# Performance work log

Hardware: AMD Instinct MI355X
Metric: run time of the kernel (lower is better)

## Reference

```python
import jax, jax.numpy as jnp
import numpy as np

N_SRC = [700000, 51200, 5120]
N_DST = [51200, 5120, 1024]
N_EDGE = [768000, 51200, 5120]
IN_FEATS, N_HIDDEN, N_CLASSES = 128, 256, 47


def setup_inputs() -> dict:
    key = jax.random.key(0)
    ks = jax.random.split(key, 16)
    inp = {}
    inp["x"] = jax.random.normal(ks[0], (N_SRC[0], IN_FEATS), dtype=jnp.float32)
    # edge lists per block: src indexes block-src nodes, dst indexes block-dst nodes
    for l in range(3):
        inp[f"src{l}"] = jax.random.randint(ks[1 + 2 * l], (N_EDGE[l],), 0, N_SRC[l], dtype=jnp.int32)
        inp[f"dst{l}"] = jax.random.randint(ks[2 + 2 * l], (N_EDGE[l],), 0, N_DST[l], dtype=jnp.int32)
    dims = [(IN_FEATS, N_HIDDEN), (N_HIDDEN, N_HIDDEN), (N_HIDDEN, N_CLASSES)]
    for l, (di, do) in enumerate(dims):
        scale = 1.0 / np.sqrt(di)
        inp[f"Ws{l}"] = jax.random.normal(ks[7 + 3 * l], (di, do), dtype=jnp.float32) * scale
        inp[f"Wn{l}"] = jax.random.normal(ks[8 + 3 * l], (di, do), dtype=jnp.float32) * scale
        inp[f"b{l}"] = jnp.zeros((do,), dtype=jnp.float32)
    return inp


def _sage_conv(h, src, dst, n_dst, Ws, Wn, b):
    # mean-aggregate neighbor (src) features onto dst nodes, then dual linear
    h_dst = h[:n_dst]                                   # dst nodes are a prefix of src nodes
    msg = jax.ops.segment_sum(h[src], dst, num_segments=n_dst)
    deg = jax.ops.segment_sum(jnp.ones((src.shape[0], 1), h.dtype), dst, num_segments=n_dst)
    h_neigh = msg / jnp.maximum(deg, 1.0)               # zero-degree dst -> 0 (DGL convention)
    return h_dst @ Ws + h_neigh @ Wn + b


def reference(x, src0, dst0, src1, dst1, src2, dst2,
              Ws0, Wn0, b0, Ws1, Wn1, b1, Ws2, Wn2, b2):
    h = _sage_conv(x, src0, dst0, N_DST[0], Ws0, Wn0, b0)
    h = jax.nn.relu(h)  # dropout = identity in eval
    h = _sage_conv(h, src1, dst1, N_DST[1], Ws1, Wn1, b1)
    h = jax.nn.relu(h)
    h = _sage_conv(h, src2, dst2, N_DST[2], Ws2, Wn2, b2)
    return h
```

## Files before the change

kernel.cpp:

```cpp
#include <hip/hip_runtime.h>


typedef __bf16 bf16x8 __attribute__((ext_vector_type(8)));
typedef float f32x4 __attribute__((ext_vector_type(4)));

static __device__ __forceinline__ unsigned short f32_to_bf16(float f) {
    unsigned u = __float_as_uint(f);
    u += 0x7fffu + ((u >> 16) & 1u);
    return (unsigned short)(u >> 16);
}
static __device__ __forceinline__ float bf16lo(unsigned u) { return __uint_as_float(u << 16); }
static __device__ __forceinline__ float bf16hi(unsigned u) { return __uint_as_float(u & 0xffff0000u); }

__global__ void sage_prep(const float* __restrict__ x, unsigned short* __restrict__ xcast,
                          const float* __restrict__ Ws0, const float* __restrict__ Wn0,
                          const float* __restrict__ Ws1, const float* __restrict__ Wn1,
                          const float* __restrict__ Ws2, const float* __restrict__ Wn2,
                          unsigned short* __restrict__ WT0, unsigned short* __restrict__ WT1,
                          unsigned short* __restrict__ WT2,
                          const int* __restrict__ d0, int* __restrict__ c0,
                          const int* __restrict__ d1, int* __restrict__ c1,
                          const int* __restrict__ d2, int* __restrict__ c2) {
    const int b = blockIdx.x;
    if (b < 6400) {
        int i = b * 256 + threadIdx.x;
        float4 v = ((const float4*)x)[i];
        uint2 o;
        o.x = (unsigned)f32_to_bf16(v.x) | ((unsigned)f32_to_bf16(v.y) << 16);
        o.y = (unsigned)f32_to_bf16(v.z) | ((unsigned)f32_to_bf16(v.w) << 16);
        ((uint2*)xcast)[i] = o;
    } else if (b < 6656) {
        int idx = (b - 6400) * 256 + threadIdx.x;
        int n = idx >> 8, k = idx & 255;
        float v = (k < 128) ? Ws0[(size_t)k * 256 + n] : Wn0[(size_t)(k - 128) * 256 + n];
        WT0[idx] = f32_to_bf16(v);
    } else if (b < 7168) {
        int idx = (b - 6656) * 256 + threadIdx.x;
        int n = idx >> 9, k = idx & 511;
        float v = (k < 256) ? Ws1[(size_t)k * 256 + n] : Wn1[(size_t)(k - 256) * 256 + n];
        WT1[idx] = f32_to_bf16(v);
    } else if (b < 7262) {
        int idx = (b - 7168) * 256 + threadIdx.x;
        int n = idx >> 9, k = idx & 511;
        float v = (k < 256) ? Ws2[(size_t)k * 47 + n] : Wn2[(size_t)(k - 256) * 47 + n];
        WT2[idx] = f32_to_bf16(v);
    } else if (b < 10262) {
        atomicAdd(&c0[d0[(b - 7262) * 256 + threadIdx.x]], 1);
    } else if (b < 10462) {
        atomicAdd(&c1[d1[(b - 10262) * 256 + threadIdx.x]], 1);
    } else {
        atomicAdd(&c2[d2[(b - 10462) * 256 + threadIdx.x]], 1);
    }
}

__global__ void sage_scan(const int* __restrict__ c0, int* __restrict__ o0, int* __restrict__ u0,
                          const int* __restrict__ c1, int* __restrict__ o1, int* __restrict__ u1,
                          const int* __restrict__ c2, int* __restrict__ o2, int* __restrict__ u2) {
    const int* counts; int* offsets; int* cursor; int n;
    if (blockIdx.x == 0)      { counts = c0; offsets = o0; cursor = u0; n = 51200; }
    else if (blockIdx.x == 1) { counts = c1; offsets = o1; cursor = u1; n = 5120; }
    else                      { counts = c2; offsets = o2; cursor = u2; n = 1024; }

    __shared__ int wsum[16];
    __shared__ int wbase[16];
    __shared__ int s_carry;
    const int tid = threadIdx.x;
    const int lane = tid & 63;
    const int wid = tid >> 6;
    if (tid == 0) s_carry = 0;
    __syncthreads();

    for (int base = 0; base < n; base += 8192) {
        int idx = base + tid * 8;
        int v[8];
#pragma unroll
        for (int u = 0; u < 8; ++u) v[u] = (idx + u < n) ? counts[idx + u] : 0;
        int tsum = 0;
#pragma unroll
        for (int u = 0; u < 8; ++u) { int t = v[u]; v[u] = tsum; tsum += t; }
        int incl = tsum;
#pragma unroll
        for (int d = 1; d < 64; d <<= 1) {
            int t = __shfl_up(incl, d, 64);
            if (lane >= d) incl += t;
        }
        int wexcl = incl - tsum;
        if (lane == 63) wsum[wid] = incl;
        __syncthreads();
        int carry = s_carry;
        __syncthreads();
        if (tid < 64) {
            int s = (lane < 16) ? wsum[lane] : 0;
            int inc = s;
#pragma unroll
            for (int d = 1; d < 16; d <<= 1) {
                int t = __shfl_up(inc, d, 64);
                if (lane >= d) inc += t;
            }
            if (lane < 16) wbase[lane] = carry + inc - s;
            if (lane == 15) s_carry = carry + inc;
        }
        __syncthreads();
        int pre = wbase[wid] + wexcl;
#pragma unroll
        for (int u = 0; u < 8; ++u)
            if (idx + u < n) { int o = pre + v[u]; offsets[idx + u] = o; cursor[idx + u] = o; }
        __syncthreads();
    }
    if (tid == 0) offsets[n] = s_carry;
}

__global__ void sage_fill(const int* __restrict__ s0, const int* __restrict__ d0,
                          int* __restrict__ u0, int* __restrict__ r0,
                          const int* __restrict__ s1, const int* __restrict__ d1,
                          int* __restrict__ u1, int* __restrict__ r1,
                          const int* __restrict__ s2, const int* __restrict__ d2,
                          int* __restrict__ u2, int* __restrict__ r2) {
    const int b = blockIdx.x;
    if (b < 3000) {
        int i = b * 256 + threadIdx.x;
        int pos = atomicAdd(&u0[d0[i]], 1);
        r0[pos] = s0[i];
    } else if (b < 3200) {
        int i = (b - 3000) * 256 + threadIdx.x;
        int pos = atomicAdd(&u1[d1[i]], 1);
        r1[pos] = s1[i];
    } else {
        int i = (b - 3200) * 256 + threadIdx.x;
        int pos = atomicAdd(&u2[d2[i]], 1);
        r2[pos] = s2[i];
    }
}

__global__ void sage_gather0(const float* __restrict__ x, const int* __restrict__ csr,
                             const int* __restrict__ off, unsigned short* __restrict__ out,
                             int n_dst) {
    int row = (blockIdx.x * 256 + threadIdx.x) >> 6;
    if (row >= n_dst) return;
    const int lane = threadIdx.x & 63;
    const int half = lane >> 5;
    const int fl = lane & 31;
    const int beg = off[row], end = off[row + 1];
    const float4* hp = (const float4*)x + fl;
    float4 accA = make_float4(0.f, 0.f, 0.f, 0.f);
    float4 accB = make_float4(0.f, 0.f, 0.f, 0.f);
    int i = beg;
    for (; i + 7 < end; i += 8) {
        int s0 = csr[i + half];
        int s1 = csr[i + 2 + half];
        int s2 = csr[i + 4 + half];
        int s3 = csr[i + 6 + half];
        float4 v0 = hp[(size_t)s0 * 32];
        float4 v1 = hp[(size_t)s1 * 32];
        float4 v2 = hp[(size_t)s2 * 32];
        float4 v3 = hp[(size_t)s3 * 32];
        accA.x += v0.x; accA.y += v0.y; accA.z += v0.z; accA.w += v0.w;
        accB.x += v1.x; accB.y += v1.y; accB.z += v1.z; accB.w += v1.w;
        accA.x += v2.x; accA.y += v2.y; accA.z += v2.z; accA.w += v2.w;
        accB.x += v3.x; accB.y += v3.y; accB.z += v3.z; accB.w += v3.w;
    }
    for (; i + 1 < end; i += 2) {
        int s = csr[i + half];
        float4 v = hp[(size_t)s * 32];
        accA.x += v.x; accA.y += v.y; accA.z += v.z; accA.w += v.w;
    }
    if (i < end && half == 0) {
        int s = csr[i];
        float4 v = hp[(size_t)s * 32];
        accA.x += v.x; accA.y += v.y; accA.z += v.z; accA.w += v.w;
    }
    accA.x += accB.x; accA.y += accB.y; accA.z += accB.z; accA.w += accB.w;
    accA.x += __shfl_down(accA.x, 32);
    accA.y += __shfl_down(accA.y, 32);
    accA.z += __shfl_down(accA.z, 32);
    accA.w += __shfl_down(accA.w, 32);
    if (half == 0) {
        float inv = 1.0f / fmaxf((float)(end - beg), 1.0f);
        uint2 o;
        o.x = (unsigned)f32_to_bf16(accA.x * inv) | ((unsigned)f32_to_bf16(accA.y * inv) << 16);
        o.y = (unsigned)f32_to_bf16(accA.z * inv) | ((unsigned)f32_to_bf16(accA.w * inv) << 16);
        ((uint2*)out)[(size_t)row * 32 + fl] = o;
    }
}

__global__ void sage_gather256(const unsigned short* __restrict__ h, const int* __restrict__ csr,
                               const int* __restrict__ off, unsigned short* __restrict__ out,
                               int n_dst) {
    int row = (blockIdx.x * 256 + threadIdx.x) >> 6;
    if (row >= n_dst) return;
    const int lane = threadIdx.x & 63;
    const int half = lane >> 5;
    const int fl = lane & 31;
    const int beg = off[row], end = off[row + 1];
    const uint4* hp = (const uint4*)h + fl;
    float a[8] = {0.f, 0.f, 0.f, 0.f, 0.f, 0.f, 0.f, 0.f};
    float b[8] = {0.f, 0.f, 0.f, 0.f, 0.f, 0.f, 0.f, 0.f};
    int i = beg;
    for (; i + 3 < end; i += 4) {
        int s0 = csr[i + half];
        int s1 = csr[i + 2 + half];
        uint4 u0 = hp[(size_t)s0 * 32];
        uint4 u1 = hp[(size_t)s1 * 32];
        a[0] += bf16lo(u0.x); a[1] += bf16hi(u0.x);
        a[2] += bf16lo(u0.y); a[3] += bf16hi(u0.y);
        a[4] += bf16lo(u0.z); a[5] += bf16hi(u0.z);
        a[6] += bf16lo(u0.w); a[7] += bf16hi(u0.w);
        b[0] += bf16lo(u1.x); b[1] += bf16hi(u1.x);
        b[2] += bf16lo(u1.y); b[3] += bf16hi(u1.y);
        b[4] += bf16lo(u1.z); b[5] += bf16hi(u1.z);
        b[6] += bf16lo(u1.w); b[7] += bf16hi(u1.w);
    }
    for (; i + 1 < end; i += 2) {
        int s = csr[i + half];
        uint4 u = hp[(size_t)s * 32];
        a[0] += bf16lo(u.x); a[1] += bf16hi(u.x);
        a[2] += bf16lo(u.y); a[3] += bf16hi(u.y);
        a[4] += bf16lo(u.z); a[5] += bf16hi(u.z);
        a[6] += bf16lo(u.w); a[7] += bf16hi(u.w);
    }
    if (i < end && half == 0) {
        int s = csr[i];
        uint4 u = hp[(size_t)s * 32];
        a[0] += bf16lo(u.x); a[1] += bf16hi(u.x);
        a[2] += bf16lo(u.y); a[3] += bf16hi(u.y);
        a[4] += bf16lo(u.z); a[5] += bf16hi(u.z);
        a[6] += bf16lo(u.w); a[7] += bf16hi(u.w);
    }
#pragma unroll
    for (int k = 0; k < 8; ++k) { a[k] += b[k]; a[k] += __shfl_down(a[k], 32); }
    if (half == 0) {
        float inv = 1.0f / fmaxf((float)(end - beg), 1.0f);
        uint4 o;
        o.x = (unsigned)f32_to_bf16(a[0] * inv) | ((unsigned)f32_to_bf16(a[1] * inv) << 16);
        o.y = (unsigned)f32_to_bf16(a[2] * inv) | ((unsigned)f32_to_bf16(a[3] * inv) << 16);
        o.z = (unsigned)f32_to_bf16(a[4] * inv) | ((unsigned)f32_to_bf16(a[5] * inv) << 16);
        o.w = (unsigned)f32_to_bf16(a[6] * inv) | ((unsigned)f32_to_bf16(a[7] * inv) << 16);
        ((uint4*)out)[(size_t)row * 32 + fl] = o;
    }
}

template <int RELU, int OUT_BF16>
__launch_bounds__(256)
__global__ void sage_gemm(const unsigned short* __restrict__ Hdst,
                          const unsigned short* __restrict__ Hneigh,
                          const unsigned short* __restrict__ WT,
                          const float* __restrict__ bias,
                          void* __restrict__ Out,
                          int N, int K1) {
    const int Ktot = 2 * K1;
    __shared__ unsigned short smem[2][128][72];
    unsigned short (*As)[72] = smem[0];
    unsigned short (*Bs)[72] = smem[1];

    const int t = threadIdx.x;
    const int lane = t & 63;
    const int w = t >> 6;
    const int wm = (w >> 1) * 64;
    const int wn = (w & 1) * 64;
    const int bm = blockIdx.y * 128;
    const int bn = blockIdx.x * 128;

    const int rowL = t >> 1;
    const int kL = (t & 1) * 32;

    f32x4 acc[4][4] = {};

    const int ktiles = Ktot >> 6;
    for (int kt = 0; kt < ktiles; ++kt) {
        const int k0 = kt << 6;
        {
            const unsigned short* src = (k0 < K1)
                ? (Hdst + (size_t)(bm + rowL) * K1 + k0 + kL)
                : (Hneigh + (size_t)(bm + rowL) * K1 + (k0 - K1) + kL);
            uint4 v0 = *(const uint4*)src;
            uint4 v1 = *(const uint4*)(src + 8);
            uint4 v2 = *(const uint4*)(src + 16);
            uint4 v3 = *(const uint4*)(src + 24);
            *(uint4*)&As[rowL][kL]      = v0;
            *(uint4*)&As[rowL][kL + 8]  = v1;
            *(uint4*)&As[rowL][kL + 16] = v2;
            *(uint4*)&As[rowL][kL + 24] = v3;
        }
        {
            int n = bn + rowL;
            uint4 v0 = {0,0,0,0}, v1 = {0,0,0,0}, v2 = {0,0,0,0}, v3 = {0,0,0,0};
            if (n < N) {
                const unsigned short* srcB = WT + (size_t)n * Ktot + k0 + kL;
                v0 = *(const uint4*)srcB;
                v1 = *(const uint4*)(srcB + 8);
                v2 = *(const uint4*)(srcB + 16);
                v3 = *(const uint4*)(srcB + 24);
            }
            *(uint4*)&Bs[rowL][kL]      = v0;
            *(uint4*)&Bs[rowL][kL + 8]  = v1;
            *(uint4*)&Bs[rowL][kL + 16] = v2;
            *(uint4*)&Bs[rowL][kL + 24] = v3;
        }
        __syncthreads();

        const int fr = lane & 15;
        const int fk = (lane >> 4) * 8;
#pragma unroll
        for (int ks = 0; ks < 64; ks += 32) {
            bf16x8 av[4], bv[4];
#pragma unroll
            for (int mt = 0; mt < 4; ++mt) av[mt] = *(const bf16x8*)&As[wm + mt * 16 + fr][ks + fk];
#pragma unroll
            for (int nt = 0; nt < 4; ++nt) bv[nt] = *(const bf16x8*)&Bs[wn + nt * 16 + fr][ks + fk];
#pragma unroll
            for (int mt = 0; mt < 4; ++mt)
#pragma unroll
                for (int nt = 0; nt < 4; ++nt)
                    acc[mt][nt] = __builtin_amdgcn_mfma_f32_16x16x32_bf16(av[mt], bv[nt], acc[mt][nt], 0, 0, 0);
        }
        __syncthreads();
    }

    const int quad = lane >> 4;
    const int colL = lane & 15;
    if (OUT_BF16 && N == 256) {
        unsigned short* C = (unsigned short*)smem;
#pragma unroll
        for (int mt = 0; mt < 4; ++mt)
#pragma unroll
            for (int nt = 0; nt < 4; ++nt)
#pragma unroll
                for (int r = 0; r < 4; ++r) {
                    int lrow = wm + mt * 16 + quad * 4 + r;
                    int lcol = wn + nt * 16 + colL;
                    float v = acc[mt][nt][r] + bias[bn + lcol];
                    if (RELU) v = fmaxf(v, 0.0f);
                    C[lrow * 136 + lcol] = f32_to_bf16(v);
                }
        __syncthreads();
        unsigned short* o = (unsigned short*)Out;
#pragma unroll
        for (int c = 0; c < 8; ++c) {
            int chunk = t * 8 + c;
            int row = chunk >> 4, cc = chunk & 15;
            uint4 v = *(const uint4*)&C[row * 136 + cc * 8];
            *(uint4*)(o + (size_t)(bm + row) * N + bn + cc * 8) = v;
        }
    } else {
#pragma unroll
        for (int mt = 0; mt < 4; ++mt)
#pragma unroll
            for (int nt = 0; nt < 4; ++nt)
#pragma unroll
                for (int r = 0; r < 4; ++r) {
                    int grow = bm + wm + mt * 16 + quad * 4 + r;
                    int gcol = bn + wn + nt * 16 + colL;
                    if (gcol < N) {
                        float v = acc[mt][nt][r] + bias[gcol];
                        if (RELU) v = fmaxf(v, 0.0f);
                        if (OUT_BF16) ((unsigned short*)Out)[(size_t)grow * N + gcol] = f32_to_bf16(v);
                        else ((float*)Out)[(size_t)grow * N + gcol] = v;
                    }
                }
    }
}


extern "C" void kernel_launch(void* const* d_in, const int* in_sizes, int n_in,
                              void* d_out, int out_size, void* d_ws, size_t ws_size,
                              hipStream_t stream) {
    const float* x    = (const float*)d_in[0];
    const int* src0 = (const int*)d_in[1];
    const int* dst0 = (const int*)d_in[2];
    const int* src1 = (const int*)d_in[3];
    const int* dst1 = (const int*)d_in[4];
    const int* src2 = (const int*)d_in[5];
    const int* dst2 = (const int*)d_in[6];
    const float* Ws0 = (const float*)d_in[7];
    const float* Wn0 = (const float*)d_in[8];
    const float* b0  = (const float*)d_in[9];
    const float* Ws1 = (const float*)d_in[10];
    const float* Wn1 = (const float*)d_in[11];
    const float* b1  = (const float*)d_in[12];
    const float* Ws2 = (const float*)d_in[13];
    const float* Wn2 = (const float*)d_in[14];
    const float* b2  = (const float*)d_in[15];
    float* out = (float*)d_out;

    char* ws = (char*)d_ws;
    unsigned short* xcast   = (unsigned short*)(ws + 0);
    unsigned short* h1      = (unsigned short*)(ws + 13107200);
    unsigned short* h2      = (unsigned short*)(ws + 39321600);
    unsigned short* hneigh0 = (unsigned short*)(ws + 41943040);
    unsigned short* hneigh1 = (unsigned short*)(ws + 55050240);
    unsigned short* hneigh2 = (unsigned short*)(ws + 57671680);
    unsigned short* WT0     = (unsigned short*)(ws + 58195968);
    unsigned short* WT1     = (unsigned short*)(ws + 58327040);
    unsigned short* WT2     = (unsigned short*)(ws + 58589184);
    int* counts0 = (int*)(ws + 58637312);
    int* counts1 = (int*)(ws + 58842112);
    int* counts2 = (int*)(ws + 58862592);
    int* off0    = (int*)(ws + 58866688);
    int* off1    = (int*)(ws + 59071504);
    int* off2    = (int*)(ws + 59092000);
    int* cur0    = (int*)(ws + 59096112);
    int* cur1    = (int*)(ws + 59300912);
    int* cur2    = (int*)(ws + 59321392);
    int* csr0    = (int*)(ws + 59325488);
    int* csr1    = (int*)(ws + 62397488);
    int* csr2    = (int*)(ws + 62602288);

    hipMemsetAsync(counts0, 0, 229376, stream);

    sage_prep<<<10482, 256, 0, stream>>>(x, xcast, Ws0, Wn0, Ws1, Wn1, Ws2, Wn2,
                                         WT0, WT1, WT2,
                                         dst0, counts0, dst1, counts1, dst2, counts2);
    sage_scan<<<3, 1024, 0, stream>>>(counts0, off0, cur0, counts1, off1, cur1, counts2, off2, cur2);
    sage_fill<<<3220, 256, 0, stream>>>(src0, dst0, cur0, csr0,
                                        src1, dst1, cur1, csr1,
                                        src2, dst2, cur2, csr2);

    sage_gather0<<<12800, 256, 0, stream>>>(x, csr0, off0, hneigh0, 51200);
    { dim3 g(2, 400); sage_gemm<1, 1><<<g, 256, 0, stream>>>(xcast, hneigh0, WT0, b0, h1, 256, 128); }

    sage_gather256<<<1280, 256, 0, stream>>>(h1, csr1, off1, hneigh1, 5120);
    { dim3 g(2, 40); sage_gemm<1, 1><<<g, 256, 0, stream>>>(h1, hneigh1, WT1, b1, h2, 256, 256); }

    sage_gather256<<<256, 256, 0, stream>>>(h2, csr2, off2, hneigh2, 1024);
    { dim3 g(1, 8); sage_gemm<0, 0><<<g, 256, 0, stream>>>(h2, hneigh2, WT2, b2, out, 47, 256); }
}
```

Baseline: 720.0 us.

## Parallelize CSR scan across blocks with atomic sync and vectorize edge loads

The three-block serial prefix scan becomes a 56-block scan. Each block scans 1024 counts, publishes its total through a global sync array, spins until all blocks arrive, then adds the totals of the blocks before it. The count and fill kernels also process two edges per thread using int2 loads, which halves their block counts. The spin barrier assumes all 56 blocks are resident at the same time, which holds on this GPU but is not guaranteed in general.

```diff
diff --git a/kernel.cpp b/kernel.cpp
--- a/kernel.cpp
+++ b/kernel.cpp
@@ -44,70 +44,87 @@
         int n = idx >> 9, k = idx & 511;
         float v = (k < 256) ? Ws2[(size_t)k * 47 + n] : Wn2[(size_t)(k - 256) * 47 + n];
         WT2[idx] = f32_to_bf16(v);
-    } else if (b < 10262) {
-        atomicAdd(&c0[d0[(b - 7262) * 256 + threadIdx.x]], 1);
-    } else if (b < 10462) {
-        atomicAdd(&c1[d1[(b - 10262) * 256 + threadIdx.x]], 1);
+    } else if (b < 8762) {
+        int i = (b - 7262) * 256 + threadIdx.x;
+        int2 d = ((const int2*)d0)[i];
+        atomicAdd(&c0[d.x], 1);
+        atomicAdd(&c0[d.y], 1);
+    } else if (b < 8862) {
+        int i = (b - 8762) * 256 + threadIdx.x;
+        int2 d = ((const int2*)d1)[i];
+        atomicAdd(&c1[d.x], 1);
+        atomicAdd(&c1[d.y], 1);
     } else {
-        atomicAdd(&c2[d2[(b - 10462) * 256 + threadIdx.x]], 1);
-    }
-}
-
+        int i = (b - 8862) * 256 + threadIdx.x;
+        int2 d = ((const int2*)d2)[i];
+        atomicAdd(&c2[d.x], 1);
+        atomicAdd(&c2[d.y], 1);
+    }
+}
+
+__launch_bounds__(1024)
 __global__ void sage_scan(const int* __restrict__ c0, int* __restrict__ o0, int* __restrict__ u0,
                           const int* __restrict__ c1, int* __restrict__ o1, int* __restrict__ u1,
-                          const int* __restrict__ c2, int* __restrict__ o2, int* __restrict__ u2) {
-    const int* counts; int* offsets; int* cursor; int n;
-    if (blockIdx.x == 0)      { counts = c0; offsets = o0; cursor = u0; n = 51200; }
-    else if (blockIdx.x == 1) { counts = c1; offsets = o1; cursor = u1; n = 5120; }
-    else                      { counts = c2; offsets = o2; cursor = u2; n = 1024; }
-
-    __shared__ int wsum[16];
-    __shared__ int wbase[16];
-    __shared__ int s_carry;
+                          const int* __restrict__ c2, int* __restrict__ o2, int* __restrict__ u2,
+                          int* __restrict__ sync) {
+    const int b = blockIdx.x;
     const int tid = threadIdx.x;
     const int lane = tid & 63;
     const int wid = tid >> 6;
-    if (tid == 0) s_carry = 0;
+    const int* counts; int* off; int* cur; int chunk, first, nblk, n;
+    if (b < 50)      { counts = c0; off = o0; cur = u0; chunk = b;      first = 0;  nblk = 50; n = 51200; }
+    else if (b < 55) { counts = c1; off = o1; cur = u1; chunk = b - 50; first = 50; nblk = 5;  n = 5120;  }
+    else             { counts = c2; off = o2; cur = u2; chunk = 0;      first = 55; nblk = 1;  n = 1024;  }
+
+    const int idx = chunk * 1024 + tid;
+    const int v = counts[idx];
+
+    int incl = v;
+#pragma unroll
+    for (int d = 1; d < 64; d <<= 1) {
+        int t = __shfl_up(incl, d, 64);
+        if (lane >= d) incl += t;
+    }
+
+    __shared__ int wsum[16];
+    __shared__ int s_base;
+    if (lane == 63) wsum[wid] = incl;
     __syncthreads();
 
-    for (int base = 0; base < n; base += 8192) {
-        int idx = base + tid * 8;
-        int v[8];
-#pragma unroll
-        for (int u = 0; u < 8; ++u) v[u] = (idx + u < n) ? counts[idx + u] : 0;
-        int tsum = 0;
-#pragma unroll
-        for (int u = 0; u < 8; ++u) { int t = v[u]; v[u] = tsum; tsum += t; }
-        int incl = tsum;
-#pragma unroll
-        for (int d = 1; d < 64; d <<= 1) {
-            int t = __shfl_up(incl, d, 64);
-            if (lane >= d) incl += t;
-        }
-        int wexcl = incl - tsum;
-        if (lane == 63) wsum[wid] = incl;
-        __syncthreads();
-        int carry = s_carry;
-        __syncthreads();
-        if (tid < 64) {
-            int s = (lane < 16) ? wsum[lane] : 0;
-            int inc = s;
-#pragma unroll
-            for (int d = 1; d < 16; d <<= 1) {
-                int t = __shfl_up(inc, d, 64);
-                if (lane >= d) inc += t;
-            }
-            if (lane < 16) wbase[lane] = carry + inc - s;
-            if (lane == 15) s_carry = carry + inc;
-        }
-        __syncthreads();
-        int pre = wbase[wid] + wexcl;
-#pragma unroll
-        for (int u = 0; u < 8; ++u)
-            if (idx + u < n) { int o = pre + v[u]; offsets[idx + u] = o; cursor[idx + u] = o; }
-        __syncthreads();
-    }
-    if (tid == 0) offsets[n] = s_carry;
+    if (tid < 64) {
+        int s = (lane < 16) ? wsum[lane] : 0;
+        int inc = s;
+#pragma unroll
+        for (int d = 1; d < 16; d <<= 1) {
+            int t = __shfl_up(inc, d, 64);
+            if (lane >= d) inc += t;
+        }
+        if (lane < 16) wsum[lane] = inc - s;
+        if (lane == 15) {
+            __hip_atomic_store(&sync[16 + b], inc, __ATOMIC_RELEASE, __HIP_MEMORY_SCOPE_AGENT);
+            __hip_atomic_fetch_add(&sync[0], 1, __ATOMIC_RELEASE, __HIP_MEMORY_SCOPE_AGENT);
+        }
+    }
+    if (tid == 0) {
+        while (__hip_atomic_load(&sync[0], __ATOMIC_ACQUIRE, __HIP_MEMORY_SCOPE_AGENT) < 56)
+            __builtin_amdgcn_s_sleep(2);
+    }
+    __syncthreads();
+
+    if (tid < 64) {
+        int p = (lane < chunk)
+            ? __hip_atomic_load(&sync[16 + first + lane], __ATOMIC_RELAXED, __HIP_MEMORY_SCOPE_AGENT)
+            : 0;
+#pragma unroll
+        for (int d = 32; d >= 1; d >>= 1) p += __shfl_down(p, d, 64);
+        if (lane == 0) s_base = p;
+    }
+    __syncthreads();
+
+    const int excl = s_base + wsum[wid] + (incl - v);
+    off[idx] = excl;
+    cur[idx] = excl;
+    if (chunk == nblk - 1 && tid == 1023) off[n] = excl + v;
 }
 
 __global__ void sage_fill(const int* __restrict__ s0, const int* __restrict__ d0,
@@ -117,18 +134,30 @@
                           const int* __restrict__ s2, const int* __restrict__ d2,
                           int* __restrict__ u2, int* __restrict__ r2) {
     const int b = blockIdx.x;
-    if (b < 3000) {
+    if (b < 1500) {
         int i = b * 256 + threadIdx.x;
-        int pos = atomicAdd(&u0[d0[i]], 1);
-        r0[pos] = s0[i];
-    } else if (b < 3200) {
-        int i = (b - 3000) * 256 + threadIdx.x;
-        int pos = atomicAdd(&u1[d1[i]], 1);
-        r1[pos] = s1[i];
+        int2 s = ((const int2*)s0)[i];
+        int2 d = ((const int2*)d0)[i];
+        int p0 = atomicAdd(&u0[d.x], 1);
+        int p1 = atomicAdd(&u0[d.y], 1);
+        r0[p0] = s.x;
+        r0[p1] = s.y;
+    } else if (b < 1600) {
+        int i = (b - 1500) * 256 + threadIdx.x;
+        int2 s = ((const int2*)s1)[i];
+        int2 d = ((const int2*)d1)[i];
+        int p0 = atomicAdd(&u1[d.x], 1);
+        int p1 = atomicAdd(&u1[d.y], 1);
+        r1[p0] = s.x;
+        r1[p1] = s.y;
     } else {
-        int i = (b - 3200) * 256 + threadIdx.x;
-        int pos = atomicAdd(&u2[d2[i]], 1);
-        r2[pos] = s2[i];
+        int i = (b - 1600) * 256 + threadIdx.x;
+        int2 s = ((const int2*)s2)[i];
+        int2 d = ((const int2*)d2)[i];
+        int p0 = atomicAdd(&u2[d.x], 1);
+        int p1 = atomicAdd(&u2[d.y], 1);
+        r2[p0] = s.x;
+        r2[p1] = s.y;
     }
 }
 
@@ -395,23 +424,25 @@
     int* counts0 = (int*)(ws + 58637312);
     int* counts1 = (int*)(ws + 58842112);
     int* counts2 = (int*)(ws + 58862592);
-    int* off0    = (int*)(ws + 58866688);
-    int* off1    = (int*)(ws + 59071504);
-    int* off2    = (int*)(ws + 59092000);
-    int* cur0    = (int*)(ws + 59096112);
-    int* cur1    = (int*)(ws + 59300912);
-    int* cur2    = (int*)(ws + 59321392);
-    int* csr0    = (int*)(ws + 59325488);
-    int* csr1    = (int*)(ws + 62397488);
-    int* csr2    = (int*)(ws + 62602288);
-
-    hipMemsetAsync(counts0, 0, 229376, stream);
-
-    sage_prep<<<10482, 256, 0, stream>>>(x, xcast, Ws0, Wn0, Ws1, Wn1, Ws2, Wn2,
-                                         WT0, WT1, WT2,
-                                         dst0, counts0, dst1, counts1, dst2, counts2);
-    sage_scan<<<3, 1024, 0, stream>>>(counts0, off0, cur0, counts1, off1, cur1, counts2, off2, cur2);
-    sage_fill<<<3220, 256, 0, stream>>>(src0, dst0, cur0, csr0,
+    int* syncp   = (int*)(ws + 58866688);
+    int* off0    = (int*)(ws + 58870784);
+    int* off1    = (int*)(ws + 59075600);
+    int* off2    = (int*)(ws + 59096096);
+    int* cur0    = (int*)(ws + 59100208);
+    int* cur1    = (int*)(ws + 59305008);
+    int* cur2    = (int*)(ws + 59325488);
+    int* csr0    = (int*)(ws + 59329584);
+    int* csr1    = (int*)(ws + 62401584);
+    int* csr2    = (int*)(ws + 62606384);
+
+    hipMemsetAsync(counts0, 0, 233472, stream);
+
+    sage_prep<<<8872, 256, 0, stream>>>(x, xcast, Ws0, Wn0, Ws1, Wn1, Ws2, Wn2,
+                                        WT0, WT1, WT2,
+                                        dst0, counts0, dst1, counts1, dst2, counts2);
+    sage_scan<<<56, 1024, 0, stream>>>(counts0, off0, cur0, counts1, off1, cur1,
+                                       counts2, off2, cur2, syncp);
+    sage_fill<<<1610, 256, 0, stream>>>(src0, dst0, cur0, csr0,
                                         src1, dst1, cur1, csr1,
                                         src2, dst2, cur2, csr2);
 
```

Measured after the change: 652.9 us (median of 2 runs). 9.3% less time.
